# Kernel tuning notes

Measured on AMD Instinct MI355X. Metric: run time of the kernel, lower is better.

The kernel has to match this reference:

```python
import jax, jax.numpy as jnp
import numpy as np

B, T, D = 2048, 60, 6
H, F, O = 64, 10, 1


def setup_inputs() -> dict:
    key = jax.random.key(0)
    ks = jax.random.split(key, 16)
    w = lambda k, shape, s=0.1: jax.random.normal(k, shape, jnp.float32) * s
    return {
        "x": jax.random.normal(ks[0], (B, T, D), jnp.float32),
        "W_i": w(ks[1], (D, H)), "U_i": w(ks[2], (H, H)), "b_i": jnp.zeros((H,), jnp.float32),
        "W_ste": w(ks[3], (D, H)), "U_ste": w(ks[4], (H, H)), "b_ste": jnp.ones((H,), jnp.float32),
        "W_fre": w(ks[5], (D, F)), "U_fre": w(ks[6], (H, F)), "b_fre": jnp.ones((F,), jnp.float32),
        "W_c": w(ks[7], (D, H)), "U_c": w(ks[8], (H, H)), "b_c": jnp.zeros((H,), jnp.float32),
        "W_o": w(ks[9], (D, H)), "U_o": w(ks[10], (H, H)), "b_o": jnp.zeros((H,), jnp.float32),
        "U_a": w(ks[11], (F, 1)), "b_a": jnp.zeros((H,), jnp.float32),
        "W_p": w(ks[12], (H, O)), "b_p": jnp.zeros((O,), jnp.float32),
    }


def _hsig(v):
    # torch.nn.Hardsigmoid: relu6(x + 3) / 6
    return jnp.clip(v / 6.0 + 0.5, 0.0, 1.0)


def reference(x, W_i, U_i, b_i, W_ste, U_ste, b_ste, W_fre, U_fre, b_fre,
              W_c, U_c, b_c, W_o, U_o, b_o, U_a, b_a, W_p, b_p):
    b, t_len, _ = x.shape
    h_dim = W_i.shape[1]
    f_dim = W_fre.shape[1]
    freq = jnp.arange(f_dim, dtype=x.dtype) / f_dim  # (F,)
    ua = U_a[:, 0]  # (F,)

    def step(carry, x_t):
        h, S_re, S_im, t = carry
        i = _hsig(x_t @ W_i + b_i + h @ U_i)              # (B,H)
        ste = _hsig(x_t @ W_ste + b_ste + h @ U_ste)      # (B,H)
        fre = _hsig(x_t @ W_fre + b_fre + h @ U_fre)      # (B,F)
        f = ste[:, :, None] * fre[:, None, :]             # (B,H,F)
        c = i * jnp.tanh(x_t @ W_c + b_c + h @ U_c)       # (B,H)
        t = t + 1.0
        omega = (2.0 * jnp.pi) * t * freq                  # (F,)
        S_re = f * S_re + c[:, :, None] * jnp.cos(omega)   # (B,H,F)
        S_im = f * S_im + c[:, :, None] * jnp.sin(omega)   # (B,H,F)
        A = S_re * S_re + S_im * S_im                      # (B,H,F)
        a = jnp.tanh(jnp.einsum('bhf,f->bh', A, ua) + b_a)
        o = _hsig(x_t @ W_o + b_o + h @ U_o)
        h = o * a
        return (h, S_re, S_im, t), None

    init = (jnp.zeros((b, h_dim), x.dtype),
            jnp.zeros((b, h_dim, f_dim), x.dtype),
            jnp.zeros((b, h_dim, f_dim), x.dtype),
            jnp.asarray(0.0, x.dtype))
    (h, _, _, _), _ = jax.lax.scan(step, init, jnp.swapaxes(x, 0, 1))
    # original returns p from the last timestep only
    return h @ W_p + b_p
```

## Files before the change

kernel.cpp:

```cpp
#include <hip/hip_runtime.h>


#define BB 2048
#define TT 60
#define DD 6
#define HH 64
#define FF 10

#define XS 968
#define HS 72

typedef short bf16x8 __attribute__((ext_vector_type(8)));
typedef float f32x4  __attribute__((ext_vector_type(4)));

__device__ __forceinline__ unsigned short f2bf(float f) {
    union { float f; unsigned u; } v; v.f = f;
    unsigned r = v.u + 0x7fffu + ((v.u >> 16) & 1u);
    return (unsigned short)(r >> 16);
}
__device__ __forceinline__ float bf2f(unsigned short b) {
    union { unsigned u; float f; } v; v.u = ((unsigned)b) << 16; return v.f;
}
__device__ __forceinline__ float hsig_f(float v) {
    return fminf(fmaxf(fmaf(v, 0.16666666666666666f, 0.5f), 0.0f), 1.0f);
}
__device__ __forceinline__ float tanh_f(float x) {
    float xc = fminf(fmaxf(x, -12.0f), 12.0f);
    float e  = __builtin_amdgcn_exp2f(xc * 2.8853900817779268f);
    return (e - 1.0f) * __builtin_amdgcn_rcpf(e + 1.0f);
}
__device__ __forceinline__ float uni(float v) {
    return __int_as_float(__builtin_amdgcn_readfirstlane(__float_as_int(v)));
}
__device__ __forceinline__ void pinv(bf16x8& v) { asm volatile("" : "+v"(v)); }

__global__ __launch_bounds__(256)
__attribute__((amdgpu_waves_per_eu(1, 1)))
void sfm_kernel(
    const float* __restrict__ x,
    const float* __restrict__ W_i,  const float* __restrict__ U_i,  const float* __restrict__ b_i,
    const float* __restrict__ W_ste,const float* __restrict__ U_ste,const float* __restrict__ b_ste,
    const float* __restrict__ W_fre,const float* __restrict__ U_fre,const float* __restrict__ b_fre,
    const float* __restrict__ W_c,  const float* __restrict__ U_c,  const float* __restrict__ b_c,
    const float* __restrict__ W_o,  const float* __restrict__ U_o,  const float* __restrict__ b_o,
    const float* __restrict__ U_a,  const float* __restrict__ b_a,
    const float* __restrict__ W_p,  const float* __restrict__ b_p,
    float* __restrict__ out)
{
    const int tid  = threadIdx.x;
    const int lane = tid & 63;
    const int wave = tid >> 6;
    const int q    = lane >> 4;
    const int n16  = lane & 15;
    const int b0   = blockIdx.x * 8;

    __shared__ __align__(16) unsigned short xsp[8 * XS];
    __shared__ __align__(16) unsigned short hhi[8 * HS];
    __shared__ __align__(16) unsigned short hlo[8 * HS];
    __shared__ __align__(16) float zbuf[4 * 64 * 12];
    __shared__ __align__(16) float frebuf[16 * 12];
    __shared__ float red[4][8];

    for (int item = tid; item < 8 * TT; item += 256) {
        const float* xg = x + (size_t)b0 * (TT * DD) + item * DD;
        const int b = item / TT, s = item - b * TT;
        unsigned short* dst = &xsp[b * XS + s * 16];
        #pragma unroll
        for (int d = 0; d < DD; ++d) {
            const float v = xg[d];
            const unsigned short hb = f2bf(v);
            dst[d]     = hb;
            dst[8 + d] = f2bf(v - bf2f(hb));
        }
        dst[6] = 0x3F80; dst[7] = 0;
        dst[14] = 0; dst[15] = 0;
    }
    for (int i = tid; i < 8 * HS; i += 256) { hhi[i] = 0; hlo[i] = 0; }

    const float* Ug = (wave == 0) ? U_i : (wave == 1) ? U_ste : (wave == 2) ? U_c : U_o;
    const float* Wg = (wave == 0) ? W_i : (wave == 1) ? W_ste : (wave == 2) ? W_c : W_o;
    const float* bg = (wave == 0) ? b_i : (wave == 1) ? b_ste : (wave == 2) ? b_c : b_o;

    bf16x8 Bh[5][3], Bl[5][3];
    #pragma unroll
    for (int t = 0; t < 5; ++t) {
        #pragma unroll
        for (int c = 0; c < 3; ++c) {
            #pragma unroll
            for (int j = 0; j < 8; ++j) {
                const int kv = c * 32 + q * 8 + j;
                float v = 0.0f;
                if (t < 4) {
                    const int n = t * 16 + n16;
                    if      (kv < 64)  v = Ug[kv * HH + n];
                    else if (kv < 70)  v = Wg[(kv - 64) * HH + n];
                    else if (kv == 70) v = bg[n];
                } else if (wave == 3 && n16 < FF) {
                    if      (kv < 64)  v = U_fre[kv * FF + n16];
                    else if (kv < 70)  v = W_fre[(kv - 64) * FF + n16];
                    else if (kv == 70) v = b_fre[n16];
                }
                const unsigned short hb = f2bf(v);
                Bh[t][c][j] = (short)hb;
                Bl[t][c][j] = (short)f2bf(v - bf2f(hb));
            }
            pinv(Bh[t][c]); pinv(Bl[t][c]);
        }
    }

    const int pb = tid & 7;
    const int pc = tid >> 3;
    const float ba0 = b_a[pc], ba1 = b_a[pc + 32];
    const float wp0 = W_p[pc], wp1 = W_p[pc + 32];
    const float bpv = uni(b_p[0]);
    float uav[FF];
    #pragma unroll
    for (int f = 0; f < FF; ++f) uav[f] = uni(U_a[f]);

    const float CBt[FF] = { 1.0f,  0.8090169943749475f,  0.30901699437494745f,
                           -0.30901699437494745f, -0.8090169943749475f, -1.0f,
                           -0.8090169943749475f, -0.30901699437494745f,
                            0.30901699437494745f,  0.8090169943749475f };
    const float SBt[FF] = { 0.0f,  0.5877852522924731f,  0.9510565162951535f,
                            0.9510565162951535f,  0.5877852522924731f,  0.0f,
                           -0.5877852522924731f, -0.9510565162951535f,
                           -0.9510565162951535f, -0.5877852522924731f };

    float Sre0[FF], Sim0[FF], Sre1[FF], Sim1[FF], cs[FF], sn[FF];
    #pragma unroll
    for (int f = 0; f < FF; ++f) {
        Sre0[f] = 0.0f; Sim0[f] = 0.0f; Sre1[f] = 0.0f; Sim1[f] = 0.0f;
        cs[f] = CBt[f]; sn[f] = SBt[f];
    }
    float h0v = 0.0f, h1v = 0.0f;

    __syncthreads();

    int sm = 0;
    for (int s = 0; s < TT; ++s) {
        const int ab = n16 & 7;
        bf16x8 Ah[3], Al[3];
        #pragma unroll
        for (int c = 0; c < 2; ++c) {
            Ah[c] = *(const bf16x8*)&hhi[ab * HS + c * 32 + q * 8];
            Al[c] = *(const bf16x8*)&hlo[ab * HS + c * 32 + q * 8];
        }
        {
            const bf16x8 xvh = *(const bf16x8*)&xsp[ab * XS + s * 16];
            const bf16x8 xvl = *(const bf16x8*)&xsp[ab * XS + s * 16 + 8];
            const bf16x8 zf = {0, 0, 0, 0, 0, 0, 0, 0};
            Ah[2] = (q == 0) ? xvh : zf;
            Al[2] = (q == 0) ? xvl : zf;
        }

        f32x4 acc[5];
        #pragma unroll
        for (int t = 0; t < 5; ++t) {
            if (t < 4 || wave == 3) {
                f32x4 a = {0.0f, 0.0f, 0.0f, 0.0f};
                #pragma unroll
                for (int c = 0; c < 3; ++c) {
                    a = __builtin_amdgcn_mfma_f32_16x16x32_bf16(Al[c], Bh[t][c], a, 0, 0, 0);
                    a = __builtin_amdgcn_mfma_f32_16x16x32_bf16(Ah[c], Bl[t][c], a, 0, 0, 0);
                    a = __builtin_amdgcn_mfma_f32_16x16x32_bf16(Ah[c], Bh[t][c], a, 0, 0, 0);
                }
                acc[t] = a;
            }
        }

        if (lane < 32) {
            #pragma unroll
            for (int t = 0; t < 4; ++t)
                *(f32x4*)&zbuf[(wave * 64 + t * 16 + n16) * 12 + q * 4] = acc[t];
            if (wave == 3 && n16 < FF)
                *(f32x4*)&frebuf[n16 * 12 + q * 4] = acc[4];
        }
        __syncthreads();

        const float zi0 = zbuf[(0 * 64 + pc) * 12 + pb], zi1 = zbuf[(0 * 64 + pc + 32) * 12 + pb];
        const float zs0 = zbuf[(1 * 64 + pc) * 12 + pb], zs1 = zbuf[(1 * 64 + pc + 32) * 12 + pb];
        const float zc0 = zbuf[(2 * 64 + pc) * 12 + pb], zc1 = zbuf[(2 * 64 + pc + 32) * 12 + pb];
        const float zo0 = zbuf[(3 * 64 + pc) * 12 + pb], zo1 = zbuf[(3 * 64 + pc + 32) * 12 + pb];
        float fr[FF];
        #pragma unroll
        for (int f = 0; f < FF; ++f) fr[f] = hsig_f(frebuf[f * 12 + pb]);

        const float i0 = hsig_f(zi0), st0 = hsig_f(zs0), o0 = hsig_f(zo0);
        const float i1 = hsig_f(zi1), st1 = hsig_f(zs1), o1 = hsig_f(zo1);
        const float c0 = i0 * tanh_f(zc0);
        const float c1 = i1 * tanh_f(zc1);

        if (sm == 0) {
            #pragma unroll
            for (int f = 0; f < FF; ++f) { cs[f] = CBt[f]; sn[f] = SBt[f]; }
        }

        float a0 = ba0, a1 = ba1;
        #pragma unroll
        for (int f = 0; f < FF; ++f) {
            const float fc0 = st0 * fr[f], fc1 = st1 * fr[f];
            Sre0[f] = fmaf(fc0, Sre0[f], c0 * cs[f]);
            Sim0[f] = fmaf(fc0, Sim0[f], c0 * sn[f]);
            Sre1[f] = fmaf(fc1, Sre1[f], c1 * cs[f]);
            Sim1[f] = fmaf(fc1, Sim1[f], c1 * sn[f]);
            const float A0 = fmaf(Sim0[f], Sim0[f], Sre0[f] * Sre0[f]);
            const float A1 = fmaf(Sim1[f], Sim1[f], Sre1[f] * Sre1[f]);
            a0 = fmaf(A0, uav[f], a0);
            a1 = fmaf(A1, uav[f], a1);
            const float cc = cs[f];
            cs[f] = fmaf(cc, CBt[f], -(sn[f] * SBt[f]));
            sn[f] = fmaf(cc, SBt[f],   sn[f] * CBt[f]);
        }
        h0v = o0 * tanh_f(a0);
        h1v = o1 * tanh_f(a1);

        {
            const unsigned short h0b = f2bf(h0v);
            const unsigned short h1b = f2bf(h1v);
            hhi[pb * HS + pc]      = h0b;
            hhi[pb * HS + pc + 32] = h1b;
            hlo[pb * HS + pc]      = f2bf(h0v - bf2f(h0b));
            hlo[pb * HS + pc + 32] = f2bf(h1v - bf2f(h1b));
        }
        if (++sm == 10) sm = 0;
        __syncthreads();
    }

    float val = fmaf(h0v, wp0, h1v * wp1);
    val += __shfl_xor(val, 8, 64);
    val += __shfl_xor(val, 16, 64);
    val += __shfl_xor(val, 32, 64);
    if ((lane >> 3) == 0) red[wave][pb] = val;
    __syncthreads();
    if (tid < 8)
        out[b0 + tid] = red[0][tid] + red[1][tid] + red[2][tid] + red[3][tid] + bpv;
}

extern "C" void kernel_launch(void* const* d_in, const int* in_sizes, int n_in,
                              void* d_out, int out_size, void* d_ws, size_t ws_size,
                              hipStream_t stream) {
    (void)in_sizes; (void)n_in; (void)d_ws; (void)ws_size; (void)out_size;
    const float* x     = (const float*)d_in[0];
    const float* W_i   = (const float*)d_in[1];
    const float* U_i   = (const float*)d_in[2];
    const float* b_i   = (const float*)d_in[3];
    const float* W_ste = (const float*)d_in[4];
    const float* U_ste = (const float*)d_in[5];
    const float* b_ste = (const float*)d_in[6];
    const float* W_fre = (const float*)d_in[7];
    const float* U_fre = (const float*)d_in[8];
    const float* b_fre = (const float*)d_in[9];
    const float* W_c   = (const float*)d_in[10];
    const float* U_c   = (const float*)d_in[11];
    const float* b_c   = (const float*)d_in[12];
    const float* W_o   = (const float*)d_in[13];
    const float* U_o   = (const float*)d_in[14];
    const float* b_o   = (const float*)d_in[15];
    const float* U_a   = (const float*)d_in[16];
    const float* b_a   = (const float*)d_in[17];
    const float* W_p   = (const float*)d_in[18];
    const float* b_p   = (const float*)d_in[19];

    sfm_kernel<<<BB / 8, 256, 0, stream>>>(
        x, W_i, U_i, b_i, W_ste, U_ste, b_ste, W_fre, U_fre, b_fre,
        W_c, U_c, b_c, W_o, U_o, b_o, U_a, b_a, W_p, b_p, (float*)d_out);
}
```

Baseline: 164.4 us.

## Halve batch rows per block to launch 512 blocks with two blocks per CU

Each block now processes 4 batch rows instead of 8, which doubles the grid to 512 blocks and gives each thread one hidden unit instead of two. The launch bounds change from one wave per EU to allowing two blocks, so more blocks can be resident on the 256 CUs and the serial recurrence has more parallel coverage. The trade-off is that half of each 16-row MFMA tile now computes duplicate rows, so matrix work per useful row doubles, and the reduction gains an extra shuffle step.

```diff
diff --git a/kernel.cpp b/kernel.cpp
--- a/kernel.cpp
+++ b/kernel.cpp
@@ -6,6 +6,7 @@
 #define DD 6
 #define HH 64
 #define FF 10
+#define NB 4
 
 #define XS 968
 #define HS 72
@@ -34,8 +35,7 @@
 }
 __device__ __forceinline__ void pinv(bf16x8& v) { asm volatile("" : "+v"(v)); }
 
-__global__ __launch_bounds__(256)
-__attribute__((amdgpu_waves_per_eu(1, 1)))
+__global__ __launch_bounds__(256, 2)
 void sfm_kernel(
     const float* __restrict__ x,
     const float* __restrict__ W_i,  const float* __restrict__ U_i,  const float* __restrict__ b_i,
@@ -52,16 +52,16 @@
     const int wave = tid >> 6;
     const int q    = lane >> 4;
     const int n16  = lane & 15;
-    const int b0   = blockIdx.x * 8;
-
-    __shared__ __align__(16) unsigned short xsp[8 * XS];
-    __shared__ __align__(16) unsigned short hhi[8 * HS];
-    __shared__ __align__(16) unsigned short hlo[8 * HS];
-    __shared__ __align__(16) float zbuf[4 * 64 * 12];
-    __shared__ __align__(16) float frebuf[16 * 12];
-    __shared__ float red[4][8];
-
-    for (int item = tid; item < 8 * TT; item += 256) {
+    const int b0   = blockIdx.x * NB;
+
+    __shared__ __align__(16) unsigned short xsp[NB * XS];
+    __shared__ __align__(16) unsigned short hhi[NB * HS];
+    __shared__ __align__(16) unsigned short hlo[NB * HS];
+    __shared__ __align__(16) float zbuf[4 * 64 * NB];
+    __shared__ __align__(16) float frebuf[16 * NB];
+    __shared__ float red[4][NB];
+
+    for (int item = tid; item < NB * TT; item += 256) {
         const float* xg = x + (size_t)b0 * (TT * DD) + item * DD;
         const int b = item / TT, s = item - b * TT;
         unsigned short* dst = &xsp[b * XS + s * 16];
@@ -75,7 +75,7 @@
         dst[6] = 0x3F80; dst[7] = 0;
         dst[14] = 0; dst[15] = 0;
     }
-    for (int i = tid; i < 8 * HS; i += 256) { hhi[i] = 0; hlo[i] = 0; }
+    for (int i = tid; i < NB * HS; i += 256) { hhi[i] = 0; hlo[i] = 0; }
 
     const float* Ug = (wave == 0) ? U_i : (wave == 1) ? U_ste : (wave == 2) ? U_c : U_o;
     const float* Wg = (wave == 0) ? W_i : (wave == 1) ? W_ste : (wave == 2) ? W_c : W_o;
@@ -108,10 +108,10 @@
         }
     }
 
-    const int pb = tid & 7;
-    const int pc = tid >> 3;
-    const float ba0 = b_a[pc], ba1 = b_a[pc + 32];
-    const float wp0 = W_p[pc], wp1 = W_p[pc + 32];
+    const int pb = tid & (NB - 1);
+    const int pc = tid >> 2;
+    const float bav = b_a[pc];
+    const float wpv = W_p[pc];
     const float bpv = uni(b_p[0]);
     float uav[FF];
     #pragma unroll
@@ -126,19 +126,18 @@
                            -0.5877852522924731f, -0.9510565162951535f,
                            -0.9510565162951535f, -0.5877852522924731f };
 
-    float Sre0[FF], Sim0[FF], Sre1[FF], Sim1[FF], cs[FF], sn[FF];
+    float Sre[FF], Sim[FF], cs[FF], sn[FF];
     #pragma unroll
     for (int f = 0; f < FF; ++f) {
-        Sre0[f] = 0.0f; Sim0[f] = 0.0f; Sre1[f] = 0.0f; Sim1[f] = 0.0f;
-        cs[f] = CBt[f]; sn[f] = SBt[f];
-    }
-    float h0v = 0.0f, h1v = 0.0f;
+        Sre[f] = 0.0f; Sim[f] = 0.0f; cs[f] = CBt[f]; sn[f] = SBt[f];
+    }
+    float hv = 0.0f;
 
     __syncthreads();
 
     int sm = 0;
     for (int s = 0; s < TT; ++s) {
-        const int ab = n16 & 7;
+        const int ab = n16 & (NB - 1);
         bf16x8 Ah[3], Al[3];
         #pragma unroll
         for (int c = 0; c < 2; ++c) {
@@ -168,71 +167,64 @@
             }
         }
 
-        if (lane < 32) {
+        if (q == 0) {
             #pragma unroll
             for (int t = 0; t < 4; ++t)
-                *(f32x4*)&zbuf[(wave * 64 + t * 16 + n16) * 12 + q * 4] = acc[t];
+                *(f32x4*)&zbuf[(wave * 64 + t * 16 + n16) * NB] = acc[t];
             if (wave == 3 && n16 < FF)
-                *(f32x4*)&frebuf[n16 * 12 + q * 4] = acc[4];
+                *(f32x4*)&frebuf[n16 * NB] = acc[4];
         }
         __syncthreads();
 
-        const float zi0 = zbuf[(0 * 64 + pc) * 12 + pb], zi1 = zbuf[(0 * 64 + pc + 32) * 12 + pb];
-        const float zs0 = zbuf[(1 * 64 + pc) * 12 + pb], zs1 = zbuf[(1 * 64 + pc + 32) * 12 + pb];
-        const float zc0 = zbuf[(2 * 64 + pc) * 12 + pb], zc1 = zbuf[(2 * 64 + pc + 32) * 12 + pb];
-        const float zo0 = zbuf[(3 * 64 + pc) * 12 + pb], zo1 = zbuf[(3 * 64 + pc + 32) * 12 + pb];
+        const float zi = zbuf[(0 * 64 + pc) * NB + pb];
+        const float zs = zbuf[(1 * 64 + pc) * NB + pb];
+        const float zc = zbuf[(2 * 64 + pc) * NB + pb];
+        const float zo = zbuf[(3 * 64 + pc) * NB + pb];
         float fr[FF];
         #pragma unroll
-        for (int f = 0; f < FF; ++f) fr[f] = hsig_f(frebuf[f * 12 + pb]);
-
-        const float i0 = hsig_f(zi0), st0 = hsig_f(zs0), o0 = hsig_f(zo0);
-        const float i1 = hsig_f(zi1), st1 = hsig_f(zs1), o1 = hsig_f(zo1);
-        const float c0 = i0 * tanh_f(zc0);
-        const float c1 = i1 * tanh_f(zc1);
+        for (int f = 0; f < FF; ++f) fr[f] = hsig_f(frebuf[f * NB + pb]);
+
+        const float iv  = hsig_f(zi);
+        const float stv = hsig_f(zs);
+        const float ov  = hsig_f(zo);
+        const float cv  = iv * tanh_f(zc);
 
         if (sm == 0) {
             #pragma unroll
             for (int f = 0; f < FF; ++f) { cs[f] = CBt[f]; sn[f] = SBt[f]; }
         }
 
-        float a0 = ba0, a1 = ba1;
+        float aacc = bav;
         #pragma unroll
         for (int f = 0; f < FF; ++f) {
-            const float fc0 = st0 * fr[f], fc1 = st1 * fr[f];
-            Sre0[f] = fmaf(fc0, Sre0[f], c0 * cs[f]);
-            Sim0[f] = fmaf(fc0, Sim0[f], c0 * sn[f]);
-            Sre1[f] = fmaf(fc1, Sre1[f], c1 * cs[f]);
-            Sim1[f] = fmaf(fc1, Sim1[f], c1 * sn[f]);
-            const float A0 = fmaf(Sim0[f], Sim0[f], Sre0[f] * Sre0[f]);
-            const float A1 = fmaf(Sim1[f], Sim1[f], Sre1[f] * Sre1[f]);
-            a0 = fmaf(A0, uav[f], a0);
-            a1 = fmaf(A1, uav[f], a1);
+            const float fc = stv * fr[f];
+            Sre[f] = fmaf(fc, Sre[f], cv * cs[f]);
+            Sim[f] = fmaf(fc, Sim[f], cv * sn[f]);
+            const float A = fmaf(Sim[f], Sim[f], Sre[f] * Sre[f]);
+            aacc = fmaf(A, uav[f], aacc);
             const float cc = cs[f];
             cs[f] = fmaf(cc, CBt[f], -(sn[f] * SBt[f]));
             sn[f] = fmaf(cc, SBt[f],   sn[f] * CBt[f]);
         }
-        h0v = o0 * tanh_f(a0);
-        h1v = o1 * tanh_f(a1);
+        hv = ov * tanh_f(aacc);
 
         {
-            const unsigned short h0b = f2bf(h0v);
-            const unsigned short h1b = f2bf(h1v);
-            hhi[pb * HS + pc]      = h0b;
-            hhi[pb * HS + pc + 32] = h1b;
-            hlo[pb * HS + pc]      = f2bf(h0v - bf2f(h0b));
-            hlo[pb * HS + pc + 32] = f2bf(h1v - bf2f(h1b));
+            const unsigned short hb = f2bf(hv);
+            hhi[pb * HS + pc] = hb;
+            hlo[pb * HS + pc] = f2bf(hv - bf2f(hb));
         }
         if (++sm == 10) sm = 0;
         __syncthreads();
     }
 
-    float val = fmaf(h0v, wp0, h1v * wp1);
+    float val = hv * wpv;
+    val += __shfl_xor(val, 4, 64);
     val += __shfl_xor(val, 8, 64);
     val += __shfl_xor(val, 16, 64);
     val += __shfl_xor(val, 32, 64);
-    if ((lane >> 3) == 0) red[wave][pb] = val;
+    if (lane < NB) red[wave][lane] = val;
     __syncthreads();
-    if (tid < 8)
+    if (tid < NB)
         out[b0 + tid] = red[0][tid] + red[1][tid] + red[2][tid] + red[3][tid] + bpv;
 }
 
@@ -261,7 +253,7 @@
     const float* W_p   = (const float*)d_in[18];
     const float* b_p   = (const float*)d_in[19];
 
-    sfm_kernel<<<BB / 8, 256, 0, stream>>>(
+    sfm_kernel<<<BB / NB, 256, 0, stream>>>(
         x, W_i, U_i, b_i, W_ste, U_ste, b_ste, W_fre, U_fre, b_fre,
         W_c, U_c, b_c, W_o, U_o, b_o, U_a, b_a, W_p, b_p, (float*)d_out);
 }
```

Measured after the change: 177.3 us. +7.8%, slower.
